# Kernel tuning notes

Hardware: AMD Instinct MI355X
Metric: run time of the kernel (lower is better)

Reference implementation:

```python
import jax, jax.numpy as jnp
import numpy as np

B, S, H, NH = 4, 2048, 1024, 16
D = H // NH  # head dim = 64


def setup_inputs() -> dict:
    key = jax.random.key(0)
    ks = jax.random.split(key, 4)
    scale = 1.0 / np.sqrt(H)
    return {
        "hidden_states": jax.random.normal(ks[0], (B, S, H), dtype=jnp.float32),
        "attention_mask": jnp.zeros((B, 1, 1, S), dtype=jnp.float32),
        "Wq": jax.random.normal(ks[1], (H, H), dtype=jnp.float32) * scale,
        "bq": jnp.zeros((H,), dtype=jnp.float32),
        "Wk": jax.random.normal(ks[2], (H, H), dtype=jnp.float32) * scale,
        "bk": jnp.zeros((H,), dtype=jnp.float32),
        "Wv": jax.random.normal(ks[3], (H, H), dtype=jnp.float32) * scale,
        "bv": jnp.zeros((H,), dtype=jnp.float32),
    }


def _split_heads(x):
    # [B, S, H] -> [B, NH, S, D]
    return x.reshape(B, S, NH, D).transpose(0, 2, 1, 3)


def reference(hidden_states, attention_mask, Wq, bq, Wk, bk, Wv, bv):
    # NOTE: faithful to source quirk: key/value projections are applied to the
    # query projection output (mixed_query_layer), not to keyvalue_states.
    mixed_q = hidden_states @ Wq.T + bq            # [B, S, H]
    q = _split_heads(mixed_q)                       # [B, NH, S, D]
    k = _split_heads(mixed_q @ Wk.T + bk)           # [B, NH, S, D]
    v = _split_heads(mixed_q @ Wv.T + bv)           # [B, NH, S, D]

    scores = jnp.einsum("bhqd,bhkd->bhqk", q, k) / jnp.sqrt(jnp.float32(D))
    scores = scores + attention_mask                # additive mask [B,1,1,S]
    probs = jax.nn.softmax(scores, axis=-1)         # dropout = identity (eval)
    ctx = jnp.einsum("bhqk,bhkd->bhqd", probs, v)   # [B, NH, S, D]
    ctx = ctx.transpose(0, 2, 1, 3).reshape(B, S, H)
    return ctx
```

## Files before the change

### kernel.cpp

```cpp
#include <hip/hip_runtime.h>
#include <stdint.h>

typedef float  f32x4  __attribute__((ext_vector_type(4)));
typedef float  f32x16 __attribute__((ext_vector_type(16)));
typedef short  s16x8  __attribute__((ext_vector_type(8)));
typedef unsigned int u32x4 __attribute__((ext_vector_type(4)));
typedef unsigned short u16;
typedef u16    u16x4 __attribute__((ext_vector_type(4)));

#define SLEN 2048
#define HDIM 1024
#define NHEAD 16
#define DHEAD 64
#define BATCH 4
#define LOG2E 1.44269504088896340736f
#define SC2   0.18033688011111772f
#define ISC2  5.5451774444795623f

__device__ __forceinline__ u16 f2bf(float f) {
  uint32_t u = __builtin_bit_cast(uint32_t, f);
  u += 0x7FFFu + ((u >> 16) & 1u);
  return (u16)(u >> 16);
}

__device__ __forceinline__ uint32_t cvtpk2(float a, float b) {
  uint32_t r;
  asm("v_cvt_pk_bf16_f32 %0, %1, %2" : "=v"(r) : "v"(a), "v"(b));
  return r;
}

__device__ __forceinline__ void gld_lds16(const void* g, void* l) {
  __builtin_amdgcn_global_load_lds(
      (const __attribute__((address_space(1))) unsigned int*)g,
      (__attribute__((address_space(3))) unsigned int*)l, 16, 0, 0);
}

__global__ __launch_bounds__(256) void prep_all(
    const float4* __restrict__ hs, const float4* __restrict__ W0,
    const float4* __restrict__ W1, const float4* __restrict__ W2,
    const float* __restrict__ mask, const float* __restrict__ bq,
    u16* __restrict__ HSb, u16* __restrict__ O0, u16* __restrict__ O1,
    u16* __restrict__ O2, float* __restrict__ m2, float* __restrict__ bqs) {
  const int bid = blockIdx.x, tid = threadIdx.x;
  if (bid < 8192) {
    int i = bid * 256 + tid;
    float4 v = hs[i];
    u16x4 o;
    o.x = f2bf(v.x); o.y = f2bf(v.y); o.z = f2bf(v.z); o.w = f2bf(v.w);
    *(u16x4*)(HSb + (size_t)i * 4) = o;
  } else if (bid < 11264) {
    int zz = (bid - 8192) >> 10;
    int i = ((bid - 8192) & 1023) * 256 + tid;
    const float4* in = zz == 0 ? W0 : (zz == 1 ? W1 : W2);
    u16* out = zz == 0 ? O0 : (zz == 1 ? O1 : O2);
    const float sc = zz == 0 ? SC2 : ISC2;
    float4 v = in[i];
    u16x4 o;
    o.x = f2bf(v.x * sc); o.y = f2bf(v.y * sc);
    o.z = f2bf(v.z * sc); o.w = f2bf(v.w * sc);
    *(u16x4*)(out + (size_t)i * 4) = o;
  } else if (bid < 11296) {
    int i = (bid - 11264) * 256 + tid;
    m2[i] = mask[i] * LOG2E;
  } else {
    int i = (bid - 11296) * 256 + tid;
    if (i < HDIM) bqs[i] = bq[i] * SC2;
  }
}

__device__ __forceinline__ void gemm_body(const u16* __restrict__ A,
                                          const u16* __restrict__ W,
                                          const float* __restrict__ bias,
                                          u16* __restrict__ C, int mode) {
  __shared__ u16 As[128 * 64];
  __shared__ u16 Bs[128 * 64];
  const int tid = threadIdx.x;
  const int lane = tid & 63;
  const int w = tid >> 6;
  const int wr = w >> 1, wc = w & 1;
  const int brow = blockIdx.y * 128;
  const int bcol = blockIdx.x * 128;
  const int l15 = lane & 15, l4 = lane >> 4;
  const int koff = l4 * 8;

  f32x4 acc[4][4];
#pragma unroll
  for (int m = 0; m < 4; ++m)
#pragma unroll
    for (int n = 0; n < 4; ++n) acc[m][n] = f32x4{0.f, 0.f, 0.f, 0.f};

  for (int kt = 0; kt < HDIM / 64; ++kt) {
    __syncthreads();
#pragma unroll
    for (int it = 0; it < 4; ++it) {
      int c = tid + it * 256;
      int r = c >> 3, c8 = c & 7;
      gld_lds16(A + (size_t)(brow + r) * HDIM + kt * 64 + c8 * 8,
                (u16*)As + (size_t)c * 8);
      gld_lds16(W + (size_t)(bcol + r) * HDIM + kt * 64 + c8 * 8,
                (u16*)Bs + (size_t)c * 8);
    }
    __syncthreads();

#pragma unroll
    for (int kk = 0; kk < 2; ++kk) {
      s16x8 af[4], bfr[4];
#pragma unroll
      for (int m = 0; m < 4; ++m)
        af[m] = *(const s16x8*)(As + (size_t)(wr * 64 + m * 16 + l15) * 64 +
                                kk * 32 + koff);
#pragma unroll
      for (int n = 0; n < 4; ++n)
        bfr[n] = *(const s16x8*)(Bs + (size_t)(wc * 64 + n * 16 + l15) * 64 +
                                 kk * 32 + koff);
#pragma unroll
      for (int m = 0; m < 4; ++m)
#pragma unroll
        for (int n = 0; n < 4; ++n)
          acc[m][n] = __builtin_amdgcn_mfma_f32_16x16x32_bf16(af[m], bfr[n],
                                                              acc[m][n], 0, 0, 0);
    }
  }

#pragma unroll
  for (int n = 0; n < 4; ++n) {
    int col = bcol + wc * 64 + n * 16 + l15;
    float bv = bias[col];
#pragma unroll
    for (int m = 0; m < 4; ++m) {
      int row0 = brow + wr * 64 + m * 16 + l4 * 4;
      if (mode == 0) {
#pragma unroll
        for (int j = 0; j < 4; ++j)
          C[(size_t)(row0 + j) * HDIM + col] = f2bf(acc[m][n][j] + bv);
      } else {
        u16x4 o;
#pragma unroll
        for (int j = 0; j < 4; ++j) o[j] = f2bf(acc[m][n][j] + bv);
        *(u16x4*)(C + (size_t)(((row0 >> 11) << 10) + col) * SLEN +
                  (row0 & (SLEN - 1))) = o;
      }
    }
  }
}

__global__ __launch_bounds__(256) void gemm_bt(const u16* __restrict__ A,
                                               const u16* __restrict__ W,
                                               const float* __restrict__ bias,
                                               u16* __restrict__ C) {
  gemm_body(A, W, bias, C, 0);
}

__global__ __launch_bounds__(256) void gemm_kv(const u16* __restrict__ A,
                                               const u16* __restrict__ Wk,
                                               const float* __restrict__ bk,
                                               u16* __restrict__ K,
                                               const u16* __restrict__ Wv,
                                               const float* __restrict__ bv,
                                               u16* __restrict__ Vt) {
  if (blockIdx.z == 0) gemm_body(A, Wk, bk, K, 0);
  else                 gemm_body(A, Wv, bv, Vt, 1);
}

__global__ __launch_bounds__(256, 4) void attn_kernel(
    const u16* __restrict__ Qs, const u16* __restrict__ Kb,
    const u16* __restrict__ Vtg, const float* __restrict__ m2g,
    float* __restrict__ out) {
  __shared__ u16 Ks[2][64 * 64];
  __shared__ u16 Vts[2][64 * 64];

  const int tid = threadIdx.x;
  const int lane = tid & 63;
  const int w = tid >> 6;
  const int bid = blockIdx.x;
  const int swz = (bid & 7) * 128 + (bid >> 3);
  const int qt = swz & 15;
  const int bh = swz >> 4;
  const int b = bh >> 4, h = bh & 15;
  const int l31 = lane & 31;
  const int h1 = lane >> 5;

  const int q0 = qt * 128 + w * 32;
  s16x8 qf[4];
  {
    const u16* qp = Qs + (size_t)(b * SLEN + q0 + l31) * HDIM + h * DHEAD + h1 * 8;
#pragma unroll
    for (int dch = 0; dch < 4; ++dch) qf[dch] = *(const s16x8*)(qp + dch * 16);
  }

  const int r0 = tid >> 3, c0 = tid & 7;
  const int cl0 = c0 ^ (r0 & 7);
  const int r1 = r0 + 32;
  const int cl1 = c0 ^ (r1 & 7);
  const u16* Kbase = Kb + (size_t)(b * SLEN) * HDIM + h * DHEAD;
  const u16* Vbase = Vtg + (size_t)bh * 64 * SLEN;
  const float* mbase = m2g + b * SLEN;

  f32x16 acc0{}, acc1{};
  float s_sm = 0.f;

  gld_lds16(Kbase + (size_t)r0 * HDIM + cl0 * 8, &Ks[0][0] + tid * 8);
  gld_lds16(Kbase + (size_t)r1 * HDIM + cl1 * 8, &Ks[0][0] + (tid + 256) * 8);
  gld_lds16(Vbase + (size_t)r0 * SLEN + cl0 * 8, &Vts[0][0] + tid * 8);
  gld_lds16(Vbase + (size_t)r1 * SLEN + cl1 * 8, &Vts[0][0] + (tid + 256) * 8);
  __syncthreads();

  int cur = 0;
  for (int kb = 0; kb < SLEN / 64; ++kb) {
    if (kb + 1 < SLEN / 64) {
      const int nb = (kb + 1) * 64;
      gld_lds16(Kbase + (size_t)(nb + r0) * HDIM + cl0 * 8,
                &Ks[cur ^ 1][0] + tid * 8);
      gld_lds16(Kbase + (size_t)(nb + r1) * HDIM + cl1 * 8,
                &Ks[cur ^ 1][0] + (tid + 256) * 8);
      gld_lds16(Vbase + (size_t)r0 * SLEN + nb + cl0 * 8,
                &Vts[cur ^ 1][0] + tid * 8);
      gld_lds16(Vbase + (size_t)r1 * SLEN + nb + cl1 * 8,
                &Vts[cur ^ 1][0] + (tid + 256) * 8);
    }
    const u16* Kc = &Ks[cur][0];
    const u16* Vc = &Vts[cur][0];

    uint32_t W[16];
#pragma unroll
    for (int kblk = 0; kblk < 2; ++kblk) {
      f32x16 sT;
#pragma unroll
      for (int g = 0; g < 4; ++g) {
        float4 mk = *(const float4*)(mbase + kb * 64 + kblk * 32 + g * 8 + h1 * 4);
        sT[4 * g + 0] = mk.x; sT[4 * g + 1] = mk.y;
        sT[4 * g + 2] = mk.z; sT[4 * g + 3] = mk.w;
      }
      __builtin_amdgcn_s_setprio(1);
#pragma unroll
      for (int dch = 0; dch < 4; ++dch) {
        const int row = kblk * 32 + l31;
        const int ch = (dch * 2 + h1) ^ (row & 7);
        s16x8 kf = *(const s16x8*)(Kc + row * 64 + ch * 8);
        sT = __builtin_amdgcn_mfma_f32_32x32x16_bf16(kf, qf[dch], sT, 0, 0, 0);
      }
      __builtin_amdgcn_s_setprio(0);
      float ts = 0.f;
#pragma unroll
      for (int g = 0; g < 4; ++g) {
        float p0 = __builtin_amdgcn_exp2f(sT[4 * g + 0]);
        float p1 = __builtin_amdgcn_exp2f(sT[4 * g + 1]);
        float p2 = __builtin_amdgcn_exp2f(sT[4 * g + 2]);
        float p3 = __builtin_amdgcn_exp2f(sT[4 * g + 3]);
        ts += (p0 + p1) + (p2 + p3);
        W[kblk * 8 + 2 * g]     = cvtpk2(p0, p1);
        W[kblk * 8 + 2 * g + 1] = cvtpk2(p2, p3);
      }
      s_sm += ts;
    }

#pragma unroll
    for (int c = 0; c < 4; ++c) {
#pragma unroll
      for (int e = 0; e < 2; ++e) {
        uint32_t a = W[4 * c + e], bb = W[4 * c + 2 + e];
        asm("v_permlane32_swap_b32 %0, %1" : "+v"(a), "+v"(bb));
        W[4 * c + e] = a;
        W[4 * c + 2 + e] = bb;
      }
    }

    __builtin_amdgcn_s_setprio(1);
#pragma unroll
    for (int c = 0; c < 4; ++c) {
      u32x4 t = {W[4 * c], W[4 * c + 1], W[4 * c + 2], W[4 * c + 3]};
      s16x8 af = __builtin_bit_cast(s16x8, t);
      const int ch = (c * 2 + h1) ^ (l31 & 7);
      s16x8 vf0 = *(const s16x8*)(Vc + l31 * 64 + ch * 8);
      s16x8 vf1 = *(const s16x8*)(Vc + (32 + l31) * 64 + ch * 8);
      acc0 = __builtin_amdgcn_mfma_f32_32x32x16_bf16(af, vf0, acc0, 0, 0, 0);
      acc1 = __builtin_amdgcn_mfma_f32_32x32x16_bf16(af, vf1, acc1, 0, 0, 0);
    }
    __builtin_amdgcn_s_setprio(0);

    __syncthreads();
    cur ^= 1;
  }

  s_sm += __shfl_xor(s_sm, 32);
  const float sinv = 1.0f / s_sm;
  const size_t obase = (size_t)(b * SLEN + q0);
#pragma unroll
  for (int r = 0; r < 16; ++r) {
    const int qr = (r & 3) + 8 * (r >> 2) + 4 * h1;
    const float si = __shfl(sinv, qr);
    float* op = out + (obase + qr) * HDIM + h * DHEAD;
    op[l31]      = acc0[r] * si;
    op[32 + l31] = acc1[r] * si;
  }
}

extern "C" void kernel_launch(void* const* d_in, const int* in_sizes, int n_in,
                              void* d_out, int out_size, void* d_ws, size_t ws_size,
                              hipStream_t stream) {
  (void)in_sizes; (void)n_in; (void)out_size; (void)ws_size;
  const float* hs   = (const float*)d_in[0];
  const float* mask = (const float*)d_in[1];
  const float* Wq   = (const float*)d_in[2];
  const float* bq   = (const float*)d_in[3];
  const float* Wk   = (const float*)d_in[4];
  const float* bk   = (const float*)d_in[5];
  const float* Wv   = (const float*)d_in[6];
  const float* bv   = (const float*)d_in[7];
  float* out = (float*)d_out;

  char* ws = (char*)d_ws;
  const size_t MTOK = (size_t)BATCH * SLEN;
  const size_t MB = 1024 * 1024;
  u16* HSb = (u16*)ws;
  u16* Wqs = (u16*)(ws + 16 * MB);
  u16* Wks = (u16*)(ws + 18 * MB);
  u16* Wvs = (u16*)(ws + 20 * MB);
  u16* Qs  = (u16*)(ws + 22 * MB);
  u16* Kb  = (u16*)(ws + 38 * MB);
  u16* Vt  = (u16*)(ws + 54 * MB);
  float* m2  = (float*)(ws + 70 * MB);
  float* bqs = m2 + MTOK;

  prep_all<<<11300, 256, 0, stream>>>((const float4*)hs, (const float4*)Wq,
                                      (const float4*)Wk, (const float4*)Wv,
                                      mask, bq, HSb, Wqs, Wks, Wvs, m2, bqs);

  dim3 gg(HDIM / 128, MTOK / 128);
  gemm_bt<<<gg, 256, 0, stream>>>(HSb, Wqs, bqs, Qs);
  dim3 gkv(HDIM / 128, MTOK / 128, 2);
  gemm_kv<<<gkv, 256, 0, stream>>>(Qs, Wks, bk, Kb, Wvs, bv, Vt);

  attn_kernel<<<BATCH * NHEAD * (SLEN / 128), 256, 0, stream>>>(Qs, Kb, Vt, m2,
                                                                out);
}
```

Before: 190.7 us.

## Skip mask loads when mask is all-zero; compute softmax row sums via MFMA

Adds a prep block that checks whether the attention mask is entirely zero and writes a flag. The attention kernel reads the flag and skips the per-tile mask loads when it is set. The softmax denominator now comes from an extra MFMA against a ones vector instead of scalar adds and shuffles. This saves global loads and VALU work at the cost of one extra MFMA per chunk. The denominator is now summed from the bf16-rounded probabilities. The mask check is a runtime test, so the general path stays correct.

After: 187.5 us. About the same (-1.7%).

```diff
diff --git a/kernel.cpp b/kernel.cpp
--- a/kernel.cpp
+++ b/kernel.cpp
@@ -40,7 +40,8 @@
     const float4* __restrict__ W1, const float4* __restrict__ W2,
     const float* __restrict__ mask, const float* __restrict__ bq,
     u16* __restrict__ HSb, u16* __restrict__ O0, u16* __restrict__ O1,
-    u16* __restrict__ O2, float* __restrict__ m2, float* __restrict__ bqs) {
+    u16* __restrict__ O2, float* __restrict__ m2, float* __restrict__ bqs,
+    float* __restrict__ flagp) {
   const int bid = blockIdx.x, tid = threadIdx.x;
   if (bid < 8192) {
     int i = bid * 256 + tid;
@@ -62,9 +63,15 @@
   } else if (bid < 11296) {
     int i = (bid - 11264) * 256 + tid;
     m2[i] = mask[i] * LOG2E;
+  } else if (bid < 11297) {
+#pragma unroll
+    for (int k = 0; k < 4; ++k) bqs[tid + k * 256] = bq[tid + k * 256] * SC2;
   } else {
-    int i = (bid - 11296) * 256 + tid;
-    if (i < HDIM) bqs[i] = bq[i] * SC2;
+    float a = 0.f;
+#pragma unroll
+    for (int k = 0; k < 32; ++k) a += __builtin_fabsf(mask[tid + k * 256]);
+    int nz = __any(a != 0.f) ? 1 : 0;
+    if ((tid & 63) == 0) flagp[tid >> 6] = (float)nz;
   }
 }
 
@@ -165,7 +172,7 @@
 __global__ __launch_bounds__(256, 4) void attn_kernel(
     const u16* __restrict__ Qs, const u16* __restrict__ Kb,
     const u16* __restrict__ Vtg, const float* __restrict__ m2g,
-    float* __restrict__ out) {
+    const float* __restrict__ flagp, float* __restrict__ out) {
   __shared__ u16 Ks[2][64 * 64];
   __shared__ u16 Vts[2][64 * 64];
 
@@ -180,6 +187,9 @@
   const int l31 = lane & 31;
   const int h1 = lane >> 5;
 
+  const float4 fl = *(const float4*)flagp;
+  const bool mz = (fl.x == 0.f && fl.y == 0.f && fl.z == 0.f && fl.w == 0.f);
+
   const int q0 = qt * 128 + w * 32;
   s16x8 qf[4];
   {
@@ -187,6 +197,10 @@
 #pragma unroll
     for (int dch = 0; dch < 4; ++dch) qf[dch] = *(const s16x8*)(qp + dch * 16);
   }
+
+  const s16x8 onesf = {(short)0x3F80, (short)0x3F80, (short)0x3F80,
+                       (short)0x3F80, (short)0x3F80, (short)0x3F80,
+                       (short)0x3F80, (short)0x3F80};
 
   const int r0 = tid >> 3, c0 = tid & 7;
   const int cl0 = c0 ^ (r0 & 7);
@@ -196,8 +210,7 @@
   const u16* Vbase = Vtg + (size_t)bh * 64 * SLEN;
   const float* mbase = m2g + b * SLEN;
 
-  f32x16 acc0{}, acc1{};
-  float s_sm = 0.f;
+  f32x16 acc0{}, acc1{}, acc_s{};
 
   gld_lds16(Kbase + (size_t)r0 * HDIM + cl0 * 8, &Ks[0][0] + tid * 8);
   gld_lds16(Kbase + (size_t)r1 * HDIM + cl1 * 8, &Ks[0][0] + (tid + 256) * 8);
@@ -225,11 +238,16 @@
 #pragma unroll
     for (int kblk = 0; kblk < 2; ++kblk) {
       f32x16 sT;
-#pragma unroll
-      for (int g = 0; g < 4; ++g) {
-        float4 mk = *(const float4*)(mbase + kb * 64 + kblk * 32 + g * 8 + h1 * 4);
-        sT[4 * g + 0] = mk.x; sT[4 * g + 1] = mk.y;
-        sT[4 * g + 2] = mk.z; sT[4 * g + 3] = mk.w;
+      if (mz) {
+        sT = f32x16{};
+      } else {
+#pragma unroll
+        for (int g = 0; g < 4; ++g) {
+          float4 mk =
+              *(const float4*)(mbase + kb * 64 + kblk * 32 + g * 8 + h1 * 4);
+          sT[4 * g + 0] = mk.x; sT[4 * g + 1] = mk.y;
+          sT[4 * g + 2] = mk.z; sT[4 * g + 3] = mk.w;
+        }
       }
       __builtin_amdgcn_s_setprio(1);
 #pragma unroll
@@ -240,18 +258,15 @@
         sT = __builtin_amdgcn_mfma_f32_32x32x16_bf16(kf, qf[dch], sT, 0, 0, 0);
       }
       __builtin_amdgcn_s_setprio(0);
-      float ts = 0.f;
 #pragma unroll
       for (int g = 0; g < 4; ++g) {
         float p0 = __builtin_amdgcn_exp2f(sT[4 * g + 0]);
         float p1 = __builtin_amdgcn_exp2f(sT[4 * g + 1]);
         float p2 = __builtin_amdgcn_exp2f(sT[4 * g + 2]);
         float p3 = __builtin_amdgcn_exp2f(sT[4 * g + 3]);
-        ts += (p0 + p1) + (p2 + p3);
         W[kblk * 8 + 2 * g]     = cvtpk2(p0, p1);
         W[kblk * 8 + 2 * g + 1] = cvtpk2(p2, p3);
       }
-      s_sm += ts;
     }
 
 #pragma unroll
@@ -275,6 +290,7 @@
       s16x8 vf1 = *(const s16x8*)(Vc + (32 + l31) * 64 + ch * 8);
       acc0 = __builtin_amdgcn_mfma_f32_32x32x16_bf16(af, vf0, acc0, 0, 0, 0);
       acc1 = __builtin_amdgcn_mfma_f32_32x32x16_bf16(af, vf1, acc1, 0, 0, 0);
+      acc_s = __builtin_amdgcn_mfma_f32_32x32x16_bf16(af, onesf, acc_s, 0, 0, 0);
     }
     __builtin_amdgcn_s_setprio(0);
 
@@ -282,13 +298,11 @@
     cur ^= 1;
   }
 
-  s_sm += __shfl_xor(s_sm, 32);
-  const float sinv = 1.0f / s_sm;
   const size_t obase = (size_t)(b * SLEN + q0);
 #pragma unroll
   for (int r = 0; r < 16; ++r) {
     const int qr = (r & 3) + 8 * (r >> 2) + 4 * h1;
-    const float si = __shfl(sinv, qr);
+    const float si = 1.0f / acc_s[r];
     float* op = out + (obase + qr) * HDIM + h * DHEAD;
     op[l31]      = acc0[r] * si;
     op[32 + l31] = acc1[r] * si;
@@ -321,10 +335,11 @@
   u16* Vt  = (u16*)(ws + 54 * MB);
   float* m2  = (float*)(ws + 70 * MB);
   float* bqs = m2 + MTOK;
-
-  prep_all<<<11300, 256, 0, stream>>>((const float4*)hs, (const float4*)Wq,
+  float* flg = bqs + 1024;
+
+  prep_all<<<11298, 256, 0, stream>>>((const float4*)hs, (const float4*)Wq,
                                       (const float4*)Wk, (const float4*)Wv,
-                                      mask, bq, HSb, Wqs, Wks, Wvs, m2, bqs);
+                                      mask, bq, HSb, Wqs, Wks, Wvs, m2, bqs, flg);
 
   dim3 gg(HDIM / 128, MTOK / 128);
   gemm_bt<<<gg, 256, 0, stream>>>(HSb, Wqs, bqs, Qs);
@@ -332,5 +347,5 @@
   gemm_kv<<<gkv, 256, 0, stream>>>(Qs, Wks, bk, Kb, Wvs, bv, Vt);
 
   attn_kernel<<<BATCH * NHEAD * (SLEN / 128), 256, 0, stream>>>(Qs, Kb, Vt, m2,
-                                                                out);
-}
+                                                                flg, out);
+}
```
